# Kernel tuning notes

Hardware: AMD Instinct MI355X
Metric: run time of the kernel (lower is better)

Reference implementation:

```python
import jax, jax.numpy as jnp
import numpy as np

N_NODES = 50000
N_EDGES = 1600000
IN_FEAT = 128
OUT_FEAT = 32
N_HEADS = 4
NEG_SLOPE = 0.2


def setup_inputs() -> dict:
    key = jax.random.key(0)
    ks = jax.random.split(key, 7)
    h = jax.random.normal(ks[0], (N_NODES, IN_FEAT), dtype=jnp.float32)
    W = jax.random.normal(ks[1], (IN_FEAT, N_HEADS * OUT_FEAT), dtype=jnp.float32) * 0.05
    attn_l = jax.random.normal(ks[2], (N_HEADS, OUT_FEAT), dtype=jnp.float32) * 0.1
    attn_r = jax.random.normal(ks[3], (N_HEADS, OUT_FEAT), dtype=jnp.float32) * 0.1
    bias = jax.random.normal(ks[4], (N_HEADS * OUT_FEAT,), dtype=jnp.float32) * 0.01
    src = jax.random.randint(ks[5], (N_EDGES,), 0, N_NODES, dtype=jnp.int32)
    dst = jax.random.randint(ks[6], (N_EDGES,), 0, N_NODES, dtype=jnp.int32)
    return {"h": h, "W": W, "attn_l": attn_l, "attn_r": attn_r, "bias": bias, "src": src, "dst": dst}


def reference(h, W, attn_l, attn_r, bias, src, dst):
    N = h.shape[0]
    H, F = attn_l.shape
    # linear projection, [N, H, F]
    feat = (h @ W).reshape(N, H, F)
    # per-node attention halves
    el = jnp.einsum('nhf,hf->nh', feat, attn_l)  # [N, H]
    er = jnp.einsum('nhf,hf->nh', feat, attn_r)  # [N, H]
    # edge scores: e_ij = leaky_relu(el[src] + er[dst])
    e = jax.nn.leaky_relu(el[src] + er[dst], negative_slope=NEG_SLOPE)  # [E, H]
    # edge softmax over incoming edges of each dst node (numerically stable)
    m = jax.ops.segment_max(e, dst, num_segments=N)  # [N, H]
    m = jnp.where(jnp.isfinite(m), m, jnp.zeros_like(m))  # zero-in-degree guard
    ex = jnp.exp(e - m[dst])  # [E, H]
    denom = jax.ops.segment_sum(ex, dst, num_segments=N)  # [N, H]
    alpha = ex / jnp.maximum(denom[dst], 1e-9)  # [E, H]
    # weighted scatter-sum aggregation
    msg = feat[src] * alpha[:, :, None]  # [E, H, F]
    rst = jax.ops.segment_sum(msg, dst, num_segments=N)  # [N, H, F]
    rst = rst + bias.reshape(1, H, F)
    rst = jax.nn.relu(rst)
    # wrapper: norm=None, dropout=0.0 (eval), mean over heads
    return jnp.mean(rst, axis=1)  # [N, F]
```

## Files before the change

kernel.cpp:

```cpp
#include <hip/hip_runtime.h>
#include <hip/hip_bf16.h>
#include <hip/hip_fp16.h>
#include <math.h>


#define NEG_SLOPE 0.2f
#define HEADS 4
#define FEAT_OUT 32
#define FEAT_ALL 128
#define IN_FEAT 128
#define KP 136
#define NBLK1 512
#define NBKT_MAX 512
#define CHE_MAX 3200
#define QCAP 2048

typedef _Float16 half8 __attribute__((ext_vector_type(8)));
typedef float float4v __attribute__((ext_vector_type(4)));
typedef unsigned int uint4v __attribute__((ext_vector_type(4)));

__device__ __forceinline__ float leaky(float v) {
    return v > 0.f ? v : NEG_SLOPE * v;
}

__global__ __launch_bounds__(256) void k1_fused(
    const int* __restrict__ src, const int* __restrict__ dst, int E,
    int che, int nbkt,
    unsigned int* __restrict__ ds, int* __restrict__ hist,
    const float* __restrict__ h, const float* __restrict__ W,
    const float* __restrict__ attn_l, const float* __restrict__ attn_r,
    unsigned char* __restrict__ feat8, float2* __restrict__ elsc,
    float* __restrict__ er, int N, int nG) {
    __shared__ _Float16 sf[64 * KP];
    const int t = threadIdx.x;

    if ((int)blockIdx.x >= nG) {
        const int blk = blockIdx.x - nG;
        int* hb = (int*)sf;
        for (int i = t; i < nbkt; i += 256) hb[i] = 0;
        __syncthreads();
        const int e_lo = blk * che;
        int e_hi = e_lo + che; if (e_hi > E) e_hi = E;
        for (int e0 = e_lo + t * 4; e0 < e_hi; e0 += 1024) {
            if (e0 + 3 < e_hi) {
                uint4v s4 = *(const uint4v*)(src + e0);
                uint4v d4 = *(const uint4v*)(dst + e0);
                uint4v r;
#pragma unroll
                for (int j = 0; j < 4; j++) r[j] = (s4[j] << 16) | d4[j];
                *(uint4v*)(ds + e0) = r;
#pragma unroll
                for (int j = 0; j < 4; j++) atomicAdd(&hb[d4[j] >> 7], 1);
            } else {
                for (int e = e0; e < e_hi; ++e) {
                    unsigned s = (unsigned)src[e], d = (unsigned)dst[e];
                    ds[e] = (s << 16) | d;
                    atomicAdd(&hb[d >> 7], 1);
                }
            }
        }
        __syncthreads();
        for (int i = t; i < nbkt; i += 256) hist[i * NBLK1 + blk] = hb[i];
        return;
    }

    const int n0 = blockIdx.x * 64;
    const int wv_ = t >> 6;
    const int lane = t & 63;
    const int m16 = lane & 15;
    const int quad = lane >> 4;
    const int rowA = wv_ * 16 + m16;
    int nA = n0 + rowA; if (nA > N - 1) nA = N - 1;
    const float* hp = h + (size_t)nA * IN_FEAT + quad * 8;

    float4v acc[8];
#pragma unroll
    for (int i = 0; i < 8; i++) acc[i] = (float4v){0.f, 0.f, 0.f, 0.f};

#pragma unroll
    for (int k0 = 0; k0 < 128; k0 += 32) {
        float4 a0 = *(const float4*)(hp + k0);
        float4 a1 = *(const float4*)(hp + k0 + 4);
        half8 a;
        a[0] = (_Float16)a0.x; a[1] = (_Float16)a0.y;
        a[2] = (_Float16)a0.z; a[3] = (_Float16)a0.w;
        a[4] = (_Float16)a1.x; a[5] = (_Float16)a1.y;
        a[6] = (_Float16)a1.z; a[7] = (_Float16)a1.w;
        const float* wp = W + (size_t)(k0 + quad * 8) * FEAT_ALL + m16;
#pragma unroll
        for (int tN = 0; tN < 8; tN++) {
            const float* wpt = wp + tN * 16;
            half8 b;
            b[0] = (_Float16)wpt[0];
            b[1] = (_Float16)wpt[FEAT_ALL];
            b[2] = (_Float16)wpt[2 * FEAT_ALL];
            b[3] = (_Float16)wpt[3 * FEAT_ALL];
            b[4] = (_Float16)wpt[4 * FEAT_ALL];
            b[5] = (_Float16)wpt[5 * FEAT_ALL];
            b[6] = (_Float16)wpt[6 * FEAT_ALL];
            b[7] = (_Float16)wpt[7 * FEAT_ALL];
            acc[tN] = __builtin_amdgcn_mfma_f32_16x16x32_f16(a, b, acc[tN], 0, 0, 0);
        }
    }

#pragma unroll
    for (int tN = 0; tN < 8; tN++)
#pragma unroll
        for (int r = 0; r < 4; r++) {
            int row = wv_ * 16 + quad * 4 + r;
            sf[row * KP + tN * 16 + m16] = (_Float16)acc[tN][r];
        }
    __syncthreads();

    {
        int r = t >> 2, hh = t & 3;
        int n = n0 + r;
        if (n < N) {
            const _Float16* sp_ = &sf[r * KP + hh * FEAT_OUT];
            float sl = 0.f, sr = 0.f, mx = 0.f;
#pragma unroll
            for (int f = 0; f < FEAT_OUT; f++) {
                float v = (float)sp_[f];
                sl += v * attn_l[hh * FEAT_OUT + f];
                sr += v * attn_r[hh * FEAT_OUT + f];
                mx = fmaxf(mx, fabsf(v));
            }
            er[n * HEADS + hh] = sr;
            elsc[n * HEADS + hh] = make_float2(sl, mx * (1.f / 127.f));
            const float inv = mx > 0.f ? 127.f / mx : 0.f;
            unsigned int w[8];
#pragma unroll
            for (int k2 = 0; k2 < 8; k2++) {
                unsigned int wv = 0;
#pragma unroll
                for (int j = 0; j < 4; j++) {
                    float v = (float)sp_[k2 * 4 + j];
                    int q = __float2int_rn(v * inv);
                    wv |= ((unsigned int)(q & 0xff)) << (8 * j);
                }
                w[k2] = wv;
            }
            uint4* dp = (uint4*)(feat8 + (size_t)n * FEAT_ALL + hh * 32);
            dp[0] = make_uint4(w[0], w[1], w[2], w[3]);
            dp[1] = make_uint4(w[4], w[5], w[6], w[7]);
        }
    }
}

__global__ __launch_bounds__(256) void s1_scan(
    const int* __restrict__ hist, int* __restrict__ base1,
    int* __restrict__ tot, int nbkt) {
    __shared__ int sm[256];
    const int b = blockIdx.x;
    const int t = threadIdx.x;
    const int v0 = hist[b * NBLK1 + 2 * t];
    const int v1 = hist[b * NBLK1 + 2 * t + 1];
    const int s = v0 + v1;
    sm[t] = s; __syncthreads();
    for (int off = 1; off < 256; off <<= 1) {
        int x = (t >= off) ? sm[t - off] : 0;
        __syncthreads();
        sm[t] += x;
        __syncthreads();
    }
    const int excl = sm[t] - s;
    base1[(2 * t) * nbkt + b] = excl;
    base1[(2 * t + 1) * nbkt + b] = excl + v0;
    if (t == 255) tot[b] = sm[255];
}

__global__ __launch_bounds__(256) void p2_place(
    const unsigned int* __restrict__ ds, const int* __restrict__ hist,
    const int* __restrict__ base1, const int* __restrict__ tot,
    unsigned int* __restrict__ srt, int E, int che, int nbkt) {
    __shared__ int cur[NBKT_MAX];
    __shared__ int gst[NBKT_MAX];
    __shared__ int bbloc[NBKT_MAX];
    __shared__ int sm[256];
    __shared__ unsigned int stage[CHE_MAX];
    __shared__ int gaddr[CHE_MAX];
    const int t = threadIdx.x;
    const int blk = blockIdx.x;
    const int e_lo = blk * che;
    int e_hi = e_lo + che; if (e_hi > E) e_hi = E;
    int cnt = e_hi - e_lo; if (cnt < 0) cnt = 0;

    {
        const int v0 = (2 * t < nbkt) ? tot[2 * t] : 0;
        const int v1 = (2 * t + 1 < nbkt) ? tot[2 * t + 1] : 0;
        const int s = v0 + v1;
        sm[t] = s; __syncthreads();
        for (int off = 1; off < 256; off <<= 1) {
            int x = (t >= off) ? sm[t - off] : 0;
            __syncthreads();
            sm[t] += x;
            __syncthreads();
        }
        const int excl = sm[t] - s;
        if (2 * t < nbkt) bbloc[2 * t] = excl;
        if (2 * t + 1 < nbkt) bbloc[2 * t + 1] = excl + v0;
    }
    __syncthreads();

    if (che <= CHE_MAX) {
        const int b0 = 2 * t, b1 = 2 * t + 1;
        const int h0 = (b0 < nbkt) ? hist[b0 * NBLK1 + blk] : 0;
        const int h1 = (b1 < nbkt) ? hist[b1 * NBLK1 + blk] : 0;
        const int s = h0 + h1;
        sm[t] = s; __syncthreads();
        for (int off = 1; off < 256; off <<= 1) {
            int x = (t >= off) ? sm[t - off] : 0;
            __syncthreads();
            sm[t] += x;
            __syncthreads();
        }
        const int excl = sm[t] - s;
        if (b0 < nbkt) {
            cur[b0] = excl;
            gst[b0] = bbloc[b0] + base1[blk * nbkt + b0] - excl;
        }
        if (b1 < nbkt) {
            cur[b1] = excl + h0;
            gst[b1] = bbloc[b1] + base1[blk * nbkt + b1] - (excl + h0);
        }
        __syncthreads();
        for (int e0 = e_lo + t * 4; e0 < e_hi; e0 += 1024) {
            if (e0 + 3 < e_hi) {
                uint4v q = *(const uint4v*)(ds + e0);
#pragma unroll
                for (int j = 0; j < 4; j++) {
                    int b = (int)(q[j] & 0xffffu) >> 7;
                    int r = atomicAdd(&cur[b], 1);
                    stage[r] = q[j];
                    gaddr[r] = gst[b] + r;
                }
            } else {
                for (int e = e0; e < e_hi; ++e) {
                    unsigned q = ds[e];
                    int b = (int)(q & 0xffffu) >> 7;
                    int r = atomicAdd(&cur[b], 1);
                    stage[r] = q;
                    gaddr[r] = gst[b] + r;
                }
            }
        }
        __syncthreads();
        for (int i = t; i < cnt; i += 256)
            srt[gaddr[i]] = stage[i];
    } else {
        for (int i = t; i < nbkt; i += 256)
            cur[i] = bbloc[i] + base1[blk * nbkt + i];
        __syncthreads();
        for (int e = e_lo + t; e < e_hi; e += 256) {
            unsigned q = ds[e];
            int b = (int)(q & 0xffffu) >> 7;
            int idx = atomicAdd(&cur[b], 1);
            srt[idx] = q;
        }
    }
}

__global__ __launch_bounds__(256) void k5_bkt(
    const unsigned int* __restrict__ srt, const int* __restrict__ tot,
    const float2* __restrict__ elsc, const float* __restrict__ er,
    const unsigned char* __restrict__ feat8, const float* __restrict__ bias,
    float* __restrict__ out, int N, int nbkt) {
    __shared__ int red[256];
    __shared__ int rowptr[33];
    __shared__ int curq[32];
    __shared__ unsigned short stage16[QCAP];
    const int t = threadIdx.x;
    const int p = blockIdx.x & 7;
    const int kk_ = blockIdx.x >> 3;
    const int b = (kk_ >> 2) * 8 + p;
    const int qtr = kk_ & 3;
    if (b >= nbkt) return;

    int partial = 0;
    for (int i = t; i < b; i += 256) partial += tot[i];
    red[t] = partial; __syncthreads();
    for (int off = 128; off > 0; off >>= 1) {
        if (t < off) red[t] += red[t + off];
        __syncthreads();
    }
    const int s0 = red[0];
    const int M = tot[b];
    const int lo = (b << 7) + qtr * 32;

    if (t < 32) curq[t] = 0;
    __syncthreads();
    for (int i = t; i < M; i += 256) {
        int u = (int)(srt[s0 + i] & 0xffffu) - lo;
        if ((unsigned)u < 32u) atomicAdd(&curq[u], 1);
    }
    __syncthreads();
    if (t == 0) {
        int acc = 0;
#pragma unroll
        for (int j = 0; j < 32; j++) { rowptr[j] = acc; acc += curq[j]; }
        rowptr[32] = acc;
    }
    __syncthreads();
    const int Mq = rowptr[32];
    const bool staged = (Mq <= QCAP);
    if (staged) {
        if (t < 32) curq[t] = rowptr[t];
        __syncthreads();
        for (int i = t; i < M; i += 256) {
            unsigned q = srt[s0 + i];
            int u = (int)(q & 0xffffu) - lo;
            if ((unsigned)u < 32u) {
                int r = atomicAdd(&curq[u], 1);
                stage16[r] = (unsigned short)(q >> 16);
            }
        }
        __syncthreads();
    }

    const int lane = t & 63;
    const int wv = t >> 6;
    const int sub4 = lane >> 4;
    const int q4 = lane & 15;
    const int hh = q4 >> 2;
    const float4 b0v = ((const float4*)bias)[q4 * 2];
    const float4 b1v = ((const float4*)bias)[q4 * 2 + 1];

    for (int kk = 0; kk < 8; kk++) {
        const int u = wv * 8 + kk;
        const int n = lo + u;
        if (n >= N) continue;
        const int rp = rowptr[u];
        const int deg = rowptr[u + 1] - rp;
        const float ernh = er[n * HEADS + hh];

        float acc[8];
#pragma unroll
        for (int j = 0; j < 8; j++) acc[j] = 0.f;
        float den = 0.f;

        if (staged) {
#pragma unroll 4
            for (int i = sub4; i < deg; i += 4) {
                int s = (int)stage16[rp + i];
                float2 es = elsc[s * HEADS + hh];
                float ex = __expf(leaky(es.x + ernh));
                uint2 uv = *(const uint2*)(feat8 + (size_t)s * FEAT_ALL + q4 * 8);
                float exs = ex * es.y;
                den += ex;
                union { uint2 v; signed char c[8]; } cv;
                cv.v = uv;
                acc[0] += exs * (float)cv.c[0];
                acc[1] += exs * (float)cv.c[1];
                acc[2] += exs * (float)cv.c[2];
                acc[3] += exs * (float)cv.c[3];
                acc[4] += exs * (float)cv.c[4];
                acc[5] += exs * (float)cv.c[5];
                acc[6] += exs * (float)cv.c[6];
                acc[7] += exs * (float)cv.c[7];
            }
        } else {
            for (int i = sub4; i < M; i += 4) {
                unsigned q = srt[s0 + i];
                if ((int)(q & 0xffffu) != n) continue;
                int s = (int)(q >> 16);
                float2 es = elsc[s * HEADS + hh];
                float ex = __expf(leaky(es.x + ernh));
                uint2 uv = *(const uint2*)(feat8 + (size_t)s * FEAT_ALL + q4 * 8);
                float exs = ex * es.y;
                den += ex;
                union { uint2 v; signed char c[8]; } cv;
                cv.v = uv;
                acc[0] += exs * (float)cv.c[0];
                acc[1] += exs * (float)cv.c[1];
                acc[2] += exs * (float)cv.c[2];
                acc[3] += exs * (float)cv.c[3];
                acc[4] += exs * (float)cv.c[4];
                acc[5] += exs * (float)cv.c[5];
                acc[6] += exs * (float)cv.c[6];
                acc[7] += exs * (float)cv.c[7];
            }
        }

#pragma unroll
        for (int j = 0; j < 8; j++) {
            acc[j] += __shfl_xor(acc[j], 16);
            acc[j] += __shfl_xor(acc[j], 32);
        }
        den += __shfl_xor(den, 16);
        den += __shfl_xor(den, 32);
        const float idh = 1.f / fmaxf(den, 1e-9f);

        float v[8];
        v[0] = fmaxf(acc[0] * idh + b0v.x, 0.f); v[1] = fmaxf(acc[1] * idh + b0v.y, 0.f);
        v[2] = fmaxf(acc[2] * idh + b0v.z, 0.f); v[3] = fmaxf(acc[3] * idh + b0v.w, 0.f);
        v[4] = fmaxf(acc[4] * idh + b1v.x, 0.f); v[5] = fmaxf(acc[5] * idh + b1v.y, 0.f);
        v[6] = fmaxf(acc[6] * idh + b1v.z, 0.f); v[7] = fmaxf(acc[7] * idh + b1v.w, 0.f);
#pragma unroll
        for (int j = 0; j < 8; j++) {
            v[j] += __shfl_xor(v[j], 4);
            v[j] += __shfl_xor(v[j], 8);
        }
        if (lane < 4) {
            float4 o0 = make_float4(v[0] * 0.25f, v[1] * 0.25f, v[2] * 0.25f, v[3] * 0.25f);
            float4 o1 = make_float4(v[4] * 0.25f, v[5] * 0.25f, v[6] * 0.25f, v[7] * 0.25f);
            float* op = out + (size_t)n * FEAT_OUT + lane * 8;
            ((float4*)op)[0] = o0;
            ((float4*)op)[1] = o1;
        }
    }
}

extern "C" void kernel_launch(void* const* d_in, const int* in_sizes, int n_in,
                              void* d_out, int out_size, void* d_ws, size_t ws_size,
                              hipStream_t stream) {
    const float* h      = (const float*)d_in[0];
    const float* W      = (const float*)d_in[1];
    const float* attn_l = (const float*)d_in[2];
    const float* attn_r = (const float*)d_in[3];
    const float* bias   = (const float*)d_in[4];
    const int*   src    = (const int*)d_in[5];
    const int*   dst    = (const int*)d_in[6];
    float* out = (float*)d_out;

    const int N = in_sizes[0] / IN_FEAT;
    const int E = in_sizes[5];
    const int nbkt = (N + 127) >> 7;
    const int che = (((E + NBLK1 - 1) / NBLK1) + 3) & ~3;

    char* w = (char*)d_ws;
    auto alloc = [&](size_t bytes) { char* r = w; w += (bytes + 255) & ~(size_t)255; return r; };
    unsigned char* feat8   = (unsigned char*)alloc((size_t)N * FEAT_ALL);
    float2*        elsc    = (float2*)alloc((size_t)N * HEADS * sizeof(float2));
    float*         er      = (float*)alloc((size_t)N * HEADS * sizeof(float));
    unsigned int*  ds      = (unsigned int*)alloc((size_t)E * 4);
    unsigned int*  srt     = (unsigned int*)alloc((size_t)E * 4);
    int*           hist    = (int*)alloc((size_t)NBLK1 * nbkt * 4);
    int*           base1   = (int*)alloc((size_t)NBLK1 * nbkt * 4);
    int*           tot     = (int*)alloc((size_t)nbkt * 4);

    const int nG = (N + 63) / 64;
    k1_fused<<<nG + NBLK1, 256, 0, stream>>>(src, dst, E, che, nbkt, ds, hist,
                                             h, W, attn_l, attn_r,
                                             feat8, elsc, er, N, nG);
    s1_scan<<<nbkt, 256, 0, stream>>>(hist, base1, tot, nbkt);
    p2_place<<<NBLK1, 256, 0, stream>>>(ds, hist, base1, tot, srt, E, che, nbkt);

    const int nqb = 8 * (((nbkt + 7) / 8) * 4);
    k5_bkt<<<nqb, 256, 0, stream>>>(srt, tot, elsc, er, feat8, bias, out, N, nbkt);
}
```

Measured before the change: 189.2 us.

## Shrink sort buckets to 32 nodes so aggregation blocks read only their own edges

Changes the counting-sort bucket width from 128 to 32 destination nodes, which yields about 1563 buckets. Histogram, scan and placement are widened to handle up to 1792 buckets (7 per thread in the scan). The aggregation kernel now maps one block to one bucket, so each block no longer scans the full 128-node bucket and filters out three quarters of the edges. The cost is larger histogram and offset arrays (512 × nbkt), more LDS in p2_place, and more s1_scan blocks.

```diff
diff --git a/kernel.cpp b/kernel.cpp
--- a/kernel.cpp
+++ b/kernel.cpp
@@ -11,7 +11,7 @@
 #define IN_FEAT 128
 #define KP 136
 #define NBLK1 512
-#define NBKT_MAX 512
+#define NBKT_MAX 1792
 #define CHE_MAX 3200
 #define QCAP 2048
 
@@ -50,12 +50,12 @@
                 for (int j = 0; j < 4; j++) r[j] = (s4[j] << 16) | d4[j];
                 *(uint4v*)(ds + e0) = r;
 #pragma unroll
-                for (int j = 0; j < 4; j++) atomicAdd(&hb[d4[j] >> 7], 1);
+                for (int j = 0; j < 4; j++) atomicAdd(&hb[d4[j] >> 5], 1);
             } else {
                 for (int e = e0; e < e_hi; ++e) {
                     unsigned s = (unsigned)src[e], d = (unsigned)dst[e];
                     ds[e] = (s << 16) | d;
-                    atomicAdd(&hb[d >> 7], 1);
+                    atomicAdd(&hb[d >> 5], 1);
                 }
             }
         }
@@ -186,42 +186,53 @@
     int cnt = e_hi - e_lo; if (cnt < 0) cnt = 0;
 
     {
-        const int v0 = (2 * t < nbkt) ? tot[2 * t] : 0;
-        const int v1 = (2 * t + 1 < nbkt) ? tot[2 * t + 1] : 0;
-        const int s = v0 + v1;
-        sm[t] = s; __syncthreads();
+        int loc[7]; int mysum = 0;
+#pragma unroll
+        for (int j = 0; j < 7; j++) {
+            const int idx = t * 7 + j;
+            const int v = (idx < nbkt) ? tot[idx] : 0;
+            loc[j] = mysum; mysum += v;
+        }
+        sm[t] = mysum; __syncthreads();
         for (int off = 1; off < 256; off <<= 1) {
             int x = (t >= off) ? sm[t - off] : 0;
             __syncthreads();
             sm[t] += x;
             __syncthreads();
         }
-        const int excl = sm[t] - s;
-        if (2 * t < nbkt) bbloc[2 * t] = excl;
-        if (2 * t + 1 < nbkt) bbloc[2 * t + 1] = excl + v0;
+        const int excl = sm[t] - mysum;
+#pragma unroll
+        for (int j = 0; j < 7; j++) {
+            const int idx = t * 7 + j;
+            if (idx < nbkt) bbloc[idx] = excl + loc[j];
+        }
     }
     __syncthreads();
 
     if (che <= CHE_MAX) {
-        const int b0 = 2 * t, b1 = 2 * t + 1;
-        const int h0 = (b0 < nbkt) ? hist[b0 * NBLK1 + blk] : 0;
-        const int h1 = (b1 < nbkt) ? hist[b1 * NBLK1 + blk] : 0;
-        const int s = h0 + h1;
-        sm[t] = s; __syncthreads();
+        int lh[7]; int hsum = 0;
+#pragma unroll
+        for (int j = 0; j < 7; j++) {
+            const int idx = t * 7 + j;
+            const int v = (idx < nbkt) ? hist[idx * NBLK1 + blk] : 0;
+            lh[j] = hsum; hsum += v;
+        }
+        sm[t] = hsum; __syncthreads();
         for (int off = 1; off < 256; off <<= 1) {
             int x = (t >= off) ? sm[t - off] : 0;
             __syncthreads();
             sm[t] += x;
             __syncthreads();
         }
-        const int excl = sm[t] - s;
-        if (b0 < nbkt) {
-            cur[b0] = excl;
-            gst[b0] = bbloc[b0] + base1[blk * nbkt + b0] - excl;
-        }
-        if (b1 < nbkt) {
-            cur[b1] = excl + h0;
-            gst[b1] = bbloc[b1] + base1[blk * nbkt + b1] - (excl + h0);
+        const int hexcl = sm[t] - hsum;
+#pragma unroll
+        for (int j = 0; j < 7; j++) {
+            const int idx = t * 7 + j;
+            if (idx < nbkt) {
+                const int c0 = hexcl + lh[j];
+                cur[idx] = c0;
+                gst[idx] = bbloc[idx] + base1[blk * nbkt + idx] - c0;
+            }
         }
         __syncthreads();
         for (int e0 = e_lo + t * 4; e0 < e_hi; e0 += 1024) {
@@ -229,7 +240,7 @@
                 uint4v q = *(const uint4v*)(ds + e0);
 #pragma unroll
                 for (int j = 0; j < 4; j++) {
-                    int b = (int)(q[j] & 0xffffu) >> 7;
+                    int b = (int)(q[j] & 0xffffu) >> 5;
                     int r = atomicAdd(&cur[b], 1);
                     stage[r] = q[j];
                     gaddr[r] = gst[b] + r;
@@ -237,7 +248,7 @@
             } else {
                 for (int e = e0; e < e_hi; ++e) {
                     unsigned q = ds[e];
-                    int b = (int)(q & 0xffffu) >> 7;
+                    int b = (int)(q & 0xffffu) >> 5;
                     int r = atomicAdd(&cur[b], 1);
                     stage[r] = q;
                     gaddr[r] = gst[b] + r;
@@ -253,7 +264,7 @@
         __syncthreads();
         for (int e = e_lo + t; e < e_hi; e += 256) {
             unsigned q = ds[e];
-            int b = (int)(q & 0xffffu) >> 7;
+            int b = (int)(q & 0xffffu) >> 5;
             int idx = atomicAdd(&cur[b], 1);
             srt[idx] = q;
         }
@@ -270,11 +281,7 @@
     __shared__ int curq[32];
     __shared__ unsigned short stage16[QCAP];
     const int t = threadIdx.x;
-    const int p = blockIdx.x & 7;
-    const int kk_ = blockIdx.x >> 3;
-    const int b = (kk_ >> 2) * 8 + p;
-    const int qtr = kk_ & 3;
-    if (b >= nbkt) return;
+    const int b = blockIdx.x;
 
     int partial = 0;
     for (int i = t; i < b; i += 256) partial += tot[i];
@@ -285,14 +292,12 @@
     }
     const int s0 = red[0];
     const int M = tot[b];
-    const int lo = (b << 7) + qtr * 32;
+    const int lo = b << 5;
 
     if (t < 32) curq[t] = 0;
     __syncthreads();
-    for (int i = t; i < M; i += 256) {
-        int u = (int)(srt[s0 + i] & 0xffffu) - lo;
-        if ((unsigned)u < 32u) atomicAdd(&curq[u], 1);
-    }
+    for (int i = t; i < M; i += 256)
+        atomicAdd(&curq[(int)(srt[s0 + i] & 0xffffu) - lo], 1);
     __syncthreads();
     if (t == 0) {
         int acc = 0;
@@ -301,18 +306,14 @@
         rowptr[32] = acc;
     }
     __syncthreads();
-    const int Mq = rowptr[32];
-    const bool staged = (Mq <= QCAP);
+    const bool staged = (M <= QCAP);
     if (staged) {
         if (t < 32) curq[t] = rowptr[t];
         __syncthreads();
         for (int i = t; i < M; i += 256) {
             unsigned q = srt[s0 + i];
-            int u = (int)(q & 0xffffu) - lo;
-            if ((unsigned)u < 32u) {
-                int r = atomicAdd(&curq[u], 1);
-                stage16[r] = (unsigned short)(q >> 16);
-            }
+            int r = atomicAdd(&curq[(int)(q & 0xffffu) - lo], 1);
+            stage16[r] = (unsigned short)(q >> 16);
         }
         __syncthreads();
     }
@@ -424,7 +425,7 @@
 
     const int N = in_sizes[0] / IN_FEAT;
     const int E = in_sizes[5];
-    const int nbkt = (N + 127) >> 7;
+    const int nbkt = (N + 31) >> 5;
     const int che = (((E + NBLK1 - 1) / NBLK1) + 3) & ~3;
 
     char* w = (char*)d_ws;
@@ -444,7 +445,5 @@
                                              feat8, elsc, er, N, nG);
     s1_scan<<<nbkt, 256, 0, stream>>>(hist, base1, tot, nbkt);
     p2_place<<<NBLK1, 256, 0, stream>>>(ds, hist, base1, tot, srt, E, che, nbkt);
-
-    const int nqb = 8 * (((nbkt + 7) / 8) * 4);
-    k5_bkt<<<nqb, 256, 0, stream>>>(srt, tot, elsc, er, feat8, bias, out, N, nbkt);
-}
+    k5_bkt<<<nbkt, 256, 0, stream>>>(srt, tot, elsc, er, feat8, bias, out, N, nbkt);
+}
```

Result: slower. 198.0 us (+4.7%).
